# Optimization experiments

Hardware: AMD Instinct MI355X
Metric: run time of the kernel (lower is better)

## Reference

```python
import jax, jax.numpy as jnp
import numpy as np

# Fixed causal graph: 32 endo nodes, each with a private 16-dim exogenous parent.
# Nodes 0..3 are roots (no endo parents); node i>=4 has endo parents {i-4..i-1}.
N_NODES = 32
ENDO = 16      # endogenous features per node
EXO = 16       # exogenous features per node
HID = 64       # hidden width (module default hidden_features=[64,64])
N_ROOTS = 4
N_PAR = 4      # endo parents for non-root nodes
IN_ROOT = EXO                      # 16
IN_INNER = N_PAR * ENDO + EXO      # 80
BATCH = 32768


def _init(key, shape, fan_in):
    return jax.random.normal(key, shape, jnp.float32) * (1.0 / np.sqrt(fan_in))


def setup_inputs() -> dict:
    key = jax.random.key(0)
    ks = jax.random.split(key, 13)
    n_in = N_NODES - N_ROOTS
    return {
        "u": jax.random.normal(ks[0], (BATCH, N_NODES * EXO), jnp.float32),
        # stacked root MLPs: [n_roots, in, out]
        "w_r1": _init(ks[1], (N_ROOTS, IN_ROOT, HID), IN_ROOT),
        "b_r1": jnp.zeros((N_ROOTS, HID), jnp.float32),
        "w_r2": _init(ks[2], (N_ROOTS, HID, HID), HID),
        "b_r2": jnp.zeros((N_ROOTS, HID), jnp.float32),
        "w_r3": _init(ks[3], (N_ROOTS, HID, ENDO), HID),
        "b_r3": jnp.zeros((N_ROOTS, ENDO), jnp.float32),
        # stacked inner MLPs: [n_inner, in, out]
        "w_i1": _init(ks[4], (n_in, IN_INNER, HID), IN_INNER),
        "b_i1": jnp.zeros((n_in, HID), jnp.float32),
        "w_i2": _init(ks[5], (n_in, HID, HID), HID),
        "b_i2": jnp.zeros((n_in, HID), jnp.float32),
        "w_i3": _init(ks[6], (n_in, HID, ENDO), HID),
        "b_i3": jnp.zeros((n_in, ENDO), jnp.float32),
    }


def _mlp(x, w1, b1, w2, b2, w3, b3):
    h = jax.nn.relu(x @ w1 + b1)
    h = jax.nn.relu(h @ w2 + b2)
    return h @ w3 + b3


def reference(u, w_r1, b_r1, w_r2, b_r2, w_r3, b_r3,
              w_i1, b_i1, w_i2, b_i2, w_i3, b_i3):
    B = u.shape[0]
    U = u.reshape(B, N_NODES, EXO)  # per-node exogenous inputs
    # Root nodes: no endo parents, vectorized over the 4 roots.
    h = jax.nn.relu(jnp.einsum("bni,nio->bno", U[:, :N_ROOTS], w_r1) + b_r1)
    h = jax.nn.relu(jnp.einsum("bnh,nho->bno", h, w_r2) + b_r2)
    root_v = jnp.einsum("bnh,nhd->bnd", h, w_r3) + b_r3  # [B, 4, ENDO]
    V = [root_v[:, i] for i in range(N_ROOTS)]
    # Non-root nodes in topological order: gather thresholded parents -> MLP.
    for i in range(N_ROOTS, N_NODES):
        j = i - N_ROOTS
        parents = jnp.concatenate(
            [(V[p] > 0.5).astype(u.dtype) for p in range(i - N_PAR, i)], axis=-1)
        inp = jnp.concatenate([parents, U[:, i]], axis=-1)  # [B, 80]
        V.append(_mlp(inp, w_i1[j], b_i1[j], w_i2[j], b_i2[j], w_i3[j], b_i3[j]))
    # forward() uses soft=True, T/W_T/W_E=None -> E is the raw logits, batched.
    return jnp.concatenate(V, axis=-1)  # [B, N_NODES*ENDO]
```

## Files before the change

kernel.cpp:

```cpp
#include <hip/hip_runtime.h>


#define BT 64

typedef __attribute__((ext_vector_type(8))) short bf16x8;
typedef __attribute__((ext_vector_type(4))) float f32x4;
#define MFMA16 __builtin_amdgcn_mfma_f32_16x16x32_bf16

#define NODE_STRIDE 33792
#define W1_SPLIT    6144
#define W2_OFF      18432
#define W2_SPLIT    4096
#define W3_OFF      30720
#define W3_SPLIT    1024

__device__ inline unsigned short bf16_rne(float x) {
    unsigned u = __float_as_uint(x);
    u += 0x7fffu + ((u >> 16) & 1u);
    return (unsigned short)(u >> 16);
}
__device__ inline float bf16_tof(unsigned short h) {
    return __uint_as_float(((unsigned)h) << 16);
}
__device__ inline void split3(float x, unsigned short& h, unsigned short& m,
                              unsigned short& l) {
    h = bf16_rne(x);
    float r = x - bf16_tof(h);
    m = bf16_rne(r);
    float r2 = r - bf16_tof(m);
    l = bf16_rne(r2);
}

__device__ inline unsigned cvt_pk_bf16(float a, float b) {
    unsigned d;
    asm("v_cvt_pk_bf16_f32 %0, %1, %2" : "=v"(d) : "v"(a), "v"(b));
    return d;
}
__device__ inline void split3_pair(float a, float b,
                                   unsigned& h, unsigned& m, unsigned& l) {
    h = cvt_pk_bf16(a, b);
    float ra = a - __uint_as_float(h << 16);
    float rb = b - __uint_as_float(h & 0xffff0000u);
    m = cvt_pk_bf16(ra, rb);
    float sa = ra - __uint_as_float(m << 16);
    float sb = rb - __uint_as_float(m & 0xffff0000u);
    l = cvt_pk_bf16(sa, sb);
}

__device__ inline int hswz(int e, int feat) {
    return (feat & 7) | ((((feat >> 3) ^ e) & 7) << 3);
}

__device__ inline void bar_lgkm() {
    asm volatile("s_waitcnt lgkmcnt(0)\n\ts_barrier" ::: "memory");
}

#define PER_NODE_ITEMS (64 * 96 + 64 * 64 + 16 * 64)

__global__ void prep_weights(const float* __restrict__ w_r1,
                             const float* __restrict__ w_r2,
                             const float* __restrict__ w_r3,
                             const float* __restrict__ w_i1,
                             const float* __restrict__ w_i2,
                             const float* __restrict__ w_i3,
                             unsigned short* __restrict__ ws) {
    int tid = blockIdx.x * 256 + threadIdx.x;
    if (tid >= 32 * PER_NODE_ITEMS) return;
    int node = tid / PER_NODE_ITEMS;
    int r = tid - node * PER_NODE_ITEMS;
    int off, stride;
    float wv = 0.0f;
    if (r < 6144) {
        int n = r / 96, k = r - n * 96;
        if (k < 64) {
            wv = (node >= 4) ? w_i1[((node - 4) * 80 + k) * 64 + n] : 0.0f;
        } else if (k < 80) {
            wv = (node < 4) ? w_r1[(node * 16 + (k - 64)) * 64 + n]
                            : w_i1[((node - 4) * 80 + k) * 64 + n];
        }
        off = n * 96 + k; stride = W1_SPLIT;
    } else if (r < 10240) {
        int r2 = r - 6144;
        int n = r2 >> 6, k = r2 & 63;
        wv = (node < 4) ? w_r2[(node * 64 + k) * 64 + n]
                        : w_i2[((node - 4) * 64 + k) * 64 + n];
        off = W2_OFF + n * 64 + k; stride = W2_SPLIT;
    } else {
        int r3 = r - 10240;
        int n = r3 >> 6, k = r3 & 63;
        wv = (node < 4) ? w_r3[(node * 64 + k) * 16 + n]
                        : w_i3[((node - 4) * 64 + k) * 16 + n];
        off = W3_OFF + n * 64 + k; stride = W3_SPLIT;
    }
    unsigned short h, m, l;
    split3(wv, h, m, l);
    unsigned short* base = ws + node * NODE_STRIDE;
    base[off] = h;
    base[off + stride] = m;
    base[off + 2 * stride] = l;
}

#define LOAD_W1(nn) do {                                                      \
    const unsigned short* Wb_ = ws + (long)(nn) * NODE_STRIDE + n1 * 96;      \
    _Pragma("unroll") for (int g_ = 0; g_ < 2; ++g_) {                        \
        const unsigned short* wp_ = Wb_ + g_ * 32 + lq * 8;                   \
        w1f[g_ * 3 + 0] = *(const bf16x8*)(wp_);                              \
        w1f[g_ * 3 + 1] = *(const bf16x8*)(wp_ + W1_SPLIT);                   \
        w1f[g_ * 3 + 2] = *(const bf16x8*)(wp_ + 2 * W1_SPLIT);               \
    }                                                                         \
    const unsigned short* we_ = Wb_ + 64 + lq * 8;                            \
    w1f[6] = *(const bf16x8*)(we_);                                           \
    w1f[7] = *(const bf16x8*)(we_ + W1_SPLIT);                                \
    w1f[8] = *(const bf16x8*)(we_ + 2 * W1_SPLIT);                            \
} while (0)

#define LOAD_W2(nn) do {                                                      \
    const unsigned short* Wb_ =                                               \
        ws + (long)(nn) * NODE_STRIDE + W2_OFF + n1 * 64;                     \
    _Pragma("unroll") for (int g_ = 0; g_ < 2; ++g_) {                        \
        const unsigned short* wp_ = Wb_ + g_ * 32 + lq * 8;                   \
        w2f[g_ * 3 + 0] = *(const bf16x8*)(wp_);                              \
        w2f[g_ * 3 + 1] = *(const bf16x8*)(wp_ + W2_SPLIT);                   \
        w2f[g_ * 3 + 2] = *(const bf16x8*)(wp_ + 2 * W2_SPLIT);               \
    }                                                                         \
} while (0)

#define LOAD_W3(nn) do {                                                      \
    const unsigned short* Wb_ =                                               \
        ws + (long)(nn) * NODE_STRIDE + W3_OFF + lr * 64;                     \
    _Pragma("unroll") for (int g_ = 0; g_ < 2; ++g_) {                        \
        const unsigned short* wp_ = Wb_ + g_ * 32 + lq * 8;                   \
        w3f[g_ * 3 + 0] = *(const bf16x8*)(wp_);                              \
        w3f[g_ * 3 + 1] = *(const bf16x8*)(wp_ + W3_SPLIT);                   \
        w3f[g_ * 3 + 2] = *(const bf16x8*)(wp_ + 2 * W3_SPLIT);               \
    }                                                                         \
} while (0)

#define STAGE_XU(uv) do {                                                     \
    unsigned hS0_, mS0_, lS0_, hS1_, mS1_, lS1_;                              \
    split3_pair((uv).x, (uv).y, hS0_, mS0_, lS0_);                            \
    split3_pair((uv).z, (uv).w, hS1_, mS1_, lS1_);                            \
    *(uint2*)&xu[0][l][4 * w] = make_uint2(hS0_, hS1_);                       \
    *(uint2*)&xu[1][l][4 * w] = make_uint2(mS0_, mS1_);                       \
    *(uint2*)&xu[2][l][4 * w] = make_uint2(lS0_, lS1_);                       \
} while (0)

__global__ __launch_bounds__(256, 2) void ncm_mfma(
    const float* __restrict__ u,
    const unsigned short* __restrict__ ws,
    const float* __restrict__ b_r1, const float* __restrict__ b_r2,
    const float* __restrict__ b_r3, const float* __restrict__ b_i1,
    const float* __restrict__ b_i2, const float* __restrict__ b_i3,
    float* __restrict__ out)
{
    __shared__ __align__(16) unsigned short ring[4][64][24];
    __shared__ __align__(16) unsigned short xu[3][64][40];
    __shared__ __align__(16) unsigned short h1s[3][64][64];
    __shared__ __align__(16) unsigned short h2s[3][64][64];

    const int tid = threadIdx.x;
    const int l   = tid & 63;
    const int w   = tid >> 6;
    const int lr  = l & 15;
    const int lq  = l >> 4;
    const int n1  = 16 * w + lr;

    const long eg = (long)blockIdx.x * BT;
    const float* u_blk = u + eg * 512;

    bf16x8 w1f[9], w2f[6], w3f[6];

    LOAD_W1(0);
    LOAD_W2(0);
    {
        float4 uv = *(const float4*)(u_blk + (long)l * 512 + w * 4);
        STAGE_XU(uv);
    }
    bar_lgkm();

    for (int i = 0; i < 32; ++i) {
        const int nn = (i < 31) ? i + 1 : 31;
        f32x4 acc[4] = {{0,0,0,0},{0,0,0,0},{0,0,0,0},{0,0,0,0}};

        LOAD_W3(i);
        float4 uN;
        if (i < 31)
            uN = *(const float4*)(u_blk + (long)l * 512 + nn * 16 + w * 4);

        if (i >= 4) {
            #pragma unroll
            for (int g = 0; g < 2; ++g) {
                const int f = g * 32 + lq * 8;
                const int slot = (i + (f >> 4)) & 3;
                #pragma unroll
                for (int m = 0; m < 4; ++m) {
                    bf16x8 ab = *(const bf16x8*)&ring[slot][m * 16 + lr][f & 15];
                    acc[m] = MFMA16(w1f[g * 3 + 0], ab, acc[m], 0, 0, 0);
                    acc[m] = MFMA16(w1f[g * 3 + 1], ab, acc[m], 0, 0, 0);
                    acc[m] = MFMA16(w1f[g * 3 + 2], ab, acc[m], 0, 0, 0);
                }
            }
        }
        {
            #pragma unroll
            for (int m = 0; m < 4; ++m) {
                bf16x8 a0 = {}, a1 = {}, a2 = {};
                if (lq < 2) {
                    const int e = m * 16 + lr;
                    a0 = *(const bf16x8*)&xu[0][e][lq * 8];
                    a1 = *(const bf16x8*)&xu[1][e][lq * 8];
                    a2 = *(const bf16x8*)&xu[2][e][lq * 8];
                }
                acc[m] = MFMA16(w1f[6], a0, acc[m], 0, 0, 0);
                acc[m] = MFMA16(w1f[7], a0, acc[m], 0, 0, 0);
                acc[m] = MFMA16(w1f[8], a0, acc[m], 0, 0, 0);
                acc[m] = MFMA16(w1f[6], a1, acc[m], 0, 0, 0);
                acc[m] = MFMA16(w1f[7], a1, acc[m], 0, 0, 0);
                acc[m] = MFMA16(w1f[8], a1, acc[m], 0, 0, 0);
                acc[m] = MFMA16(w1f[6], a2, acc[m], 0, 0, 0);
                acc[m] = MFMA16(w1f[7], a2, acc[m], 0, 0, 0);
            }
        }
        {
            const float* B1 = (i < 4) ? (b_r1 + i * 64) : (b_i1 + (i - 4) * 64);
            float4 bv = *(const float4*)(B1 + 16 * w + 4 * lq);
            const int fo = 16 * w + 4 * lq;
            #pragma unroll
            for (int m = 0; m < 4; ++m) {
                const int e = m * 16 + lr;
                float v0 = fmaxf(acc[m][0] + bv.x, 0.0f);
                float v1 = fmaxf(acc[m][1] + bv.y, 0.0f);
                float v2 = fmaxf(acc[m][2] + bv.z, 0.0f);
                float v3 = fmaxf(acc[m][3] + bv.w, 0.0f);
                unsigned hP0, mP0, lP0, hP1, mP1, lP1;
                split3_pair(v0, v1, hP0, mP0, lP0);
                split3_pair(v2, v3, hP1, mP1, lP1);
                const int o = hswz(e, fo);
                *(uint2*)&h1s[0][e][o] = make_uint2(hP0, hP1);
                *(uint2*)&h1s[1][e][o] = make_uint2(mP0, mP1);
                *(uint2*)&h1s[2][e][o] = make_uint2(lP0, lP1);
            }
        }
        bar_lgkm();

        LOAD_W1(nn);
        if (i < 31) STAGE_XU(uN);

        #pragma unroll
        for (int m = 0; m < 4; ++m) acc[m] = (f32x4){0, 0, 0, 0};
        {
            #pragma unroll
            for (int g = 0; g < 2; ++g) {
                const int f = g * 32 + lq * 8;
                #pragma unroll
                for (int m = 0; m < 4; ++m) {
                    const int e = m * 16 + lr;
                    const int o = hswz(e, f);
                    bf16x8 a0 = *(const bf16x8*)&h1s[0][e][o];
                    bf16x8 a1 = *(const bf16x8*)&h1s[1][e][o];
                    bf16x8 a2 = *(const bf16x8*)&h1s[2][e][o];
                    acc[m] = MFMA16(w2f[g * 3 + 0], a0, acc[m], 0, 0, 0);
                    acc[m] = MFMA16(w2f[g * 3 + 1], a0, acc[m], 0, 0, 0);
                    acc[m] = MFMA16(w2f[g * 3 + 2], a0, acc[m], 0, 0, 0);
                    acc[m] = MFMA16(w2f[g * 3 + 0], a1, acc[m], 0, 0, 0);
                    acc[m] = MFMA16(w2f[g * 3 + 1], a1, acc[m], 0, 0, 0);
                    acc[m] = MFMA16(w2f[g * 3 + 2], a1, acc[m], 0, 0, 0);
                    acc[m] = MFMA16(w2f[g * 3 + 0], a2, acc[m], 0, 0, 0);
                    acc[m] = MFMA16(w2f[g * 3 + 1], a2, acc[m], 0, 0, 0);
                }
            }
        }
        {
            const float* B2 = (i < 4) ? (b_r2 + i * 64) : (b_i2 + (i - 4) * 64);
            float4 bv = *(const float4*)(B2 + 16 * w + 4 * lq);
            const int fo = 16 * w + 4 * lq;
            #pragma unroll
            for (int m = 0; m < 4; ++m) {
                const int e = m * 16 + lr;
                float v0 = fmaxf(acc[m][0] + bv.x, 0.0f);
                float v1 = fmaxf(acc[m][1] + bv.y, 0.0f);
                float v2 = fmaxf(acc[m][2] + bv.z, 0.0f);
                float v3 = fmaxf(acc[m][3] + bv.w, 0.0f);
                unsigned hP0, mP0, lP0, hP1, mP1, lP1;
                split3_pair(v0, v1, hP0, mP0, lP0);
                split3_pair(v2, v3, hP1, mP1, lP1);
                const int o = hswz(e, fo);
                *(uint2*)&h2s[0][e][o] = make_uint2(hP0, hP1);
                *(uint2*)&h2s[1][e][o] = make_uint2(mP0, mP1);
                *(uint2*)&h2s[2][e][o] = make_uint2(lP0, lP1);
            }
        }
        bar_lgkm();

        LOAD_W2(nn);
        {
            f32x4 c3 = {0, 0, 0, 0};
            const int e = 16 * w + lr;
            #pragma unroll
            for (int g = 0; g < 2; ++g) {
                const int f = g * 32 + lq * 8;
                const int o = hswz(e, f);
                bf16x8 a0 = *(const bf16x8*)&h2s[0][e][o];
                bf16x8 a1 = *(const bf16x8*)&h2s[1][e][o];
                bf16x8 a2 = *(const bf16x8*)&h2s[2][e][o];
                c3 = MFMA16(w3f[g * 3 + 0], a0, c3, 0, 0, 0);
                c3 = MFMA16(w3f[g * 3 + 1], a0, c3, 0, 0, 0);
                c3 = MFMA16(w3f[g * 3 + 2], a0, c3, 0, 0, 0);
                c3 = MFMA16(w3f[g * 3 + 0], a1, c3, 0, 0, 0);
                c3 = MFMA16(w3f[g * 3 + 1], a1, c3, 0, 0, 0);
                c3 = MFMA16(w3f[g * 3 + 2], a1, c3, 0, 0, 0);
                c3 = MFMA16(w3f[g * 3 + 0], a2, c3, 0, 0, 0);
                c3 = MFMA16(w3f[g * 3 + 1], a2, c3, 0, 0, 0);
            }
            const float* B3 = (i < 4) ? (b_r3 + i * 16) : (b_i3 + (i - 4) * 16);
            float4 bv = *(const float4*)(B3 + 4 * lq);
            float v0 = c3[0] + bv.x;
            float v1 = c3[1] + bv.y;
            float v2 = c3[2] + bv.z;
            float v3 = c3[3] + bv.w;
            *(float4*)(out + (eg + e) * 512 + i * 16 + 4 * lq) =
                make_float4(v0, v1, v2, v3);
            const int slot = i & 3;
            unsigned r0 = (v0 > 0.5f ? 0x3F80u : 0u) |
                          ((v1 > 0.5f ? 0x3F80u : 0u) << 16);
            unsigned r1 = (v2 > 0.5f ? 0x3F80u : 0u) |
                          ((v3 > 0.5f ? 0x3F80u : 0u) << 16);
            *(uint2*)&ring[slot][e][4 * lq] = make_uint2(r0, r1);
        }
        bar_lgkm();
    }
}

extern "C" void kernel_launch(void* const* d_in, const int* in_sizes, int n_in,
                              void* d_out, int out_size, void* d_ws, size_t ws_size,
                              hipStream_t stream) {
    const float* u    = (const float*)d_in[0];
    const float* w_r1 = (const float*)d_in[1];
    const float* b_r1 = (const float*)d_in[2];
    const float* w_r2 = (const float*)d_in[3];
    const float* b_r2 = (const float*)d_in[4];
    const float* w_r3 = (const float*)d_in[5];
    const float* b_r3 = (const float*)d_in[6];
    const float* w_i1 = (const float*)d_in[7];
    const float* b_i1 = (const float*)d_in[8];
    const float* w_i2 = (const float*)d_in[9];
    const float* b_i2 = (const float*)d_in[10];
    const float* w_i3 = (const float*)d_in[11];
    const float* b_i3 = (const float*)d_in[12];
    float* out = (float*)d_out;
    unsigned short* ws = (unsigned short*)d_ws;

    prep_weights<<<dim3((32 * PER_NODE_ITEMS) / 256), dim3(256), 0, stream>>>(
        w_r1, w_r2, w_r3, w_i1, w_i2, w_i3, ws);

    ncm_mfma<<<dim3(512), dim3(256), 0, stream>>>(
        u, ws, b_r1, b_r2, b_r3, b_i1, b_i2, b_i3, out);
}
```

Baseline: 284.4 us.

## Split batch rows across 8 waves per block instead of 4

Doubles the block to 512 threads. Waves are split into 4 output-column tiles times 2 batch-row halves, so each wave handles 2 row-tiles instead of 4 in layers 1 and 2. Layer 3 runs only on the first 4 waves, and each wave stages half as much exogenous input. The goal is more waves to hide MFMA and LDS latency, at the cost of duplicated weight-fragment loads per wave and idle waves during layer 3. The launch bound asks for 4 blocks per CU, which may force register pressure or spills.

New measurement: 376.0 us. 1.32x slower.

```diff
diff --git a/kernel.cpp b/kernel.cpp
--- a/kernel.cpp
+++ b/kernel.cpp
@@ -137,15 +137,14 @@
 } while (0)
 
 #define STAGE_XU(uv) do {                                                     \
-    unsigned hS0_, mS0_, lS0_, hS1_, mS1_, lS1_;                              \
-    split3_pair((uv).x, (uv).y, hS0_, mS0_, lS0_);                            \
-    split3_pair((uv).z, (uv).w, hS1_, mS1_, lS1_);                            \
-    *(uint2*)&xu[0][l][4 * w] = make_uint2(hS0_, hS1_);                       \
-    *(uint2*)&xu[1][l][4 * w] = make_uint2(mS0_, mS1_);                       \
-    *(uint2*)&xu[2][l][4 * w] = make_uint2(lS0_, lS1_);                       \
+    unsigned hS_, mS_, lS_;                                                   \
+    split3_pair((uv).x, (uv).y, hS_, mS_, lS_);                               \
+    *(unsigned*)&xu[0][l][2 * w8] = hS_;                                      \
+    *(unsigned*)&xu[1][l][2 * w8] = mS_;                                      \
+    *(unsigned*)&xu[2][l][2 * w8] = lS_;                                      \
 } while (0)
 
-__global__ __launch_bounds__(256, 2) void ncm_mfma(
+__global__ __launch_bounds__(512, 4) void ncm_mfma(
     const float* __restrict__ u,
     const unsigned short* __restrict__ ws,
     const float* __restrict__ b_r1, const float* __restrict__ b_r2,
@@ -160,10 +159,12 @@
 
     const int tid = threadIdx.x;
     const int l   = tid & 63;
-    const int w   = tid >> 6;
+    const int w8  = tid >> 6;
     const int lr  = l & 15;
     const int lq  = l >> 4;
-    const int n1  = 16 * w + lr;
+    const int nt  = w8 & 3;
+    const int mh  = w8 >> 2;
+    const int n1  = 16 * nt + lr;
 
     const long eg = (long)blockIdx.x * BT;
     const float* u_blk = u + eg * 512;
@@ -173,19 +174,19 @@
     LOAD_W1(0);
     LOAD_W2(0);
     {
-        float4 uv = *(const float4*)(u_blk + (long)l * 512 + w * 4);
+        float2 uv = *(const float2*)(u_blk + (long)l * 512 + 2 * w8);
         STAGE_XU(uv);
     }
     bar_lgkm();
 
     for (int i = 0; i < 32; ++i) {
         const int nn = (i < 31) ? i + 1 : 31;
-        f32x4 acc[4] = {{0,0,0,0},{0,0,0,0},{0,0,0,0},{0,0,0,0}};
-
-        LOAD_W3(i);
-        float4 uN;
+        f32x4 acc[2] = {{0,0,0,0},{0,0,0,0}};
+
+        if (w8 < 4) LOAD_W3(i);
+        float2 uN;
         if (i < 31)
-            uN = *(const float4*)(u_blk + (long)l * 512 + nn * 16 + w * 4);
+            uN = *(const float2*)(u_blk + (long)l * 512 + nn * 16 + 2 * w8);
 
         if (i >= 4) {
             #pragma unroll
@@ -193,8 +194,9 @@
                 const int f = g * 32 + lq * 8;
                 const int slot = (i + (f >> 4)) & 3;
                 #pragma unroll
-                for (int m = 0; m < 4; ++m) {
-                    bf16x8 ab = *(const bf16x8*)&ring[slot][m * 16 + lr][f & 15];
+                for (int m = 0; m < 2; ++m) {
+                    const int e = (2 * mh + m) * 16 + lr;
+                    bf16x8 ab = *(const bf16x8*)&ring[slot][e][f & 15];
                     acc[m] = MFMA16(w1f[g * 3 + 0], ab, acc[m], 0, 0, 0);
                     acc[m] = MFMA16(w1f[g * 3 + 1], ab, acc[m], 0, 0, 0);
                     acc[m] = MFMA16(w1f[g * 3 + 2], ab, acc[m], 0, 0, 0);
@@ -203,10 +205,10 @@
         }
         {
             #pragma unroll
-            for (int m = 0; m < 4; ++m) {
+            for (int m = 0; m < 2; ++m) {
                 bf16x8 a0 = {}, a1 = {}, a2 = {};
                 if (lq < 2) {
-                    const int e = m * 16 + lr;
+                    const int e = (2 * mh + m) * 16 + lr;
                     a0 = *(const bf16x8*)&xu[0][e][lq * 8];
                     a1 = *(const bf16x8*)&xu[1][e][lq * 8];
                     a2 = *(const bf16x8*)&xu[2][e][lq * 8];
@@ -223,11 +225,11 @@
         }
         {
             const float* B1 = (i < 4) ? (b_r1 + i * 64) : (b_i1 + (i - 4) * 64);
-            float4 bv = *(const float4*)(B1 + 16 * w + 4 * lq);
-            const int fo = 16 * w + 4 * lq;
-            #pragma unroll
-            for (int m = 0; m < 4; ++m) {
-                const int e = m * 16 + lr;
+            float4 bv = *(const float4*)(B1 + 16 * nt + 4 * lq);
+            const int fo = 16 * nt + 4 * lq;
+            #pragma unroll
+            for (int m = 0; m < 2; ++m) {
+                const int e = (2 * mh + m) * 16 + lr;
                 float v0 = fmaxf(acc[m][0] + bv.x, 0.0f);
                 float v1 = fmaxf(acc[m][1] + bv.y, 0.0f);
                 float v2 = fmaxf(acc[m][2] + bv.z, 0.0f);
@@ -247,14 +249,14 @@
         if (i < 31) STAGE_XU(uN);
 
         #pragma unroll
-        for (int m = 0; m < 4; ++m) acc[m] = (f32x4){0, 0, 0, 0};
+        for (int m = 0; m < 2; ++m) acc[m] = (f32x4){0, 0, 0, 0};
         {
             #pragma unroll
             for (int g = 0; g < 2; ++g) {
                 const int f = g * 32 + lq * 8;
                 #pragma unroll
-                for (int m = 0; m < 4; ++m) {
-                    const int e = m * 16 + lr;
+                for (int m = 0; m < 2; ++m) {
+                    const int e = (2 * mh + m) * 16 + lr;
                     const int o = hswz(e, f);
                     bf16x8 a0 = *(const bf16x8*)&h1s[0][e][o];
                     bf16x8 a1 = *(const bf16x8*)&h1s[1][e][o];
@@ -272,11 +274,11 @@
         }
         {
             const float* B2 = (i < 4) ? (b_r2 + i * 64) : (b_i2 + (i - 4) * 64);
-            float4 bv = *(const float4*)(B2 + 16 * w + 4 * lq);
-            const int fo = 16 * w + 4 * lq;
-            #pragma unroll
-            for (int m = 0; m < 4; ++m) {
-                const int e = m * 16 + lr;
+            float4 bv = *(const float4*)(B2 + 16 * nt + 4 * lq);
+            const int fo = 16 * nt + 4 * lq;
+            #pragma unroll
+            for (int m = 0; m < 2; ++m) {
+                const int e = (2 * mh + m) * 16 + lr;
                 float v0 = fmaxf(acc[m][0] + bv.x, 0.0f);
                 float v1 = fmaxf(acc[m][1] + bv.y, 0.0f);
                 float v2 = fmaxf(acc[m][2] + bv.z, 0.0f);
@@ -293,9 +295,9 @@
         bar_lgkm();
 
         LOAD_W2(nn);
-        {
+        if (w8 < 4) {
             f32x4 c3 = {0, 0, 0, 0};
-            const int e = 16 * w + lr;
+            const int e = 16 * w8 + lr;
             #pragma unroll
             for (int g = 0; g < 2; ++g) {
                 const int f = g * 32 + lq * 8;
@@ -353,6 +355,6 @@
     prep_weights<<<dim3((32 * PER_NODE_ITEMS) / 256), dim3(256), 0, stream>>>(
         w_r1, w_r2, w_r3, w_i1, w_i2, w_i3, ws);
 
-    ncm_mfma<<<dim3(512), dim3(256), 0, stream>>>(
+    ncm_mfma<<<dim3(512), dim3(512), 0, stream>>>(
         u, ws, b_r1, b_r2, b_r3, b_i1, b_i2, b_i3, out);
 }
```

## Make each wave own its batch rows in layer 2 to drop a barrier

Applied to the files above, without the earlier changes.

Layer 2 is repartitioned so each wave computes all 64 hidden outputs for its own 16 batch rows, instead of 16 outputs for all 64 rows. Layer 3 then reads only h2 rows the same wave wrote, so the block barrier between layer 2 and layer 3 is removed. The cost is holding all of W2 in registers per wave (24 bf16x8 fragments instead of 6), which raises register pressure and global weight load traffic and may lower occupancy.

New measurement: 420.4 us. +47.8%, slower.

```diff
diff --git a/kernel.cpp b/kernel.cpp
--- a/kernel.cpp
+++ b/kernel.cpp
@@ -115,13 +115,15 @@
 } while (0)
 
 #define LOAD_W2(nn) do {                                                      \
-    const unsigned short* Wb_ =                                               \
-        ws + (long)(nn) * NODE_STRIDE + W2_OFF + n1 * 64;                     \
-    _Pragma("unroll") for (int g_ = 0; g_ < 2; ++g_) {                        \
-        const unsigned short* wp_ = Wb_ + g_ * 32 + lq * 8;                   \
-        w2f[g_ * 3 + 0] = *(const bf16x8*)(wp_);                              \
-        w2f[g_ * 3 + 1] = *(const bf16x8*)(wp_ + W2_SPLIT);                   \
-        w2f[g_ * 3 + 2] = *(const bf16x8*)(wp_ + 2 * W2_SPLIT);               \
+    _Pragma("unroll") for (int nt_ = 0; nt_ < 4; ++nt_) {                     \
+        const unsigned short* Wb_ = ws + (long)(nn) * NODE_STRIDE + W2_OFF    \
+                                    + (nt_ * 16 + lr) * 64;                   \
+        _Pragma("unroll") for (int g_ = 0; g_ < 2; ++g_) {                    \
+            const unsigned short* wp_ = Wb_ + g_ * 32 + lq * 8;               \
+            w2f[nt_ * 6 + g_ * 3 + 0] = *(const bf16x8*)(wp_);                \
+            w2f[nt_ * 6 + g_ * 3 + 1] = *(const bf16x8*)(wp_ + W2_SPLIT);     \
+            w2f[nt_ * 6 + g_ * 3 + 2] = *(const bf16x8*)(wp_ + 2 * W2_SPLIT); \
+        }                                                                     \
     }                                                                         \
 } while (0)
 
@@ -164,11 +166,12 @@
     const int lr  = l & 15;
     const int lq  = l >> 4;
     const int n1  = 16 * w + lr;
+    const int e2  = 16 * w + lr;
 
     const long eg = (long)blockIdx.x * BT;
     const float* u_blk = u + eg * 512;
 
-    bf16x8 w1f[9], w2f[6], w3f[6];
+    bf16x8 w1f[9], w2f[24], w3f[6];
 
     LOAD_W1(0);
     LOAD_W2(0);
@@ -252,57 +255,51 @@
             #pragma unroll
             for (int g = 0; g < 2; ++g) {
                 const int f = g * 32 + lq * 8;
+                const int o = hswz(e2, f);
+                bf16x8 a0 = *(const bf16x8*)&h1s[0][e2][o];
+                bf16x8 a1 = *(const bf16x8*)&h1s[1][e2][o];
+                bf16x8 a2 = *(const bf16x8*)&h1s[2][e2][o];
                 #pragma unroll
-                for (int m = 0; m < 4; ++m) {
-                    const int e = m * 16 + lr;
-                    const int o = hswz(e, f);
-                    bf16x8 a0 = *(const bf16x8*)&h1s[0][e][o];
-                    bf16x8 a1 = *(const bf16x8*)&h1s[1][e][o];
-                    bf16x8 a2 = *(const bf16x8*)&h1s[2][e][o];
-                    acc[m] = MFMA16(w2f[g * 3 + 0], a0, acc[m], 0, 0, 0);
-                    acc[m] = MFMA16(w2f[g * 3 + 1], a0, acc[m], 0, 0, 0);
-                    acc[m] = MFMA16(w2f[g * 3 + 2], a0, acc[m], 0, 0, 0);
-                    acc[m] = MFMA16(w2f[g * 3 + 0], a1, acc[m], 0, 0, 0);
-                    acc[m] = MFMA16(w2f[g * 3 + 1], a1, acc[m], 0, 0, 0);
-                    acc[m] = MFMA16(w2f[g * 3 + 2], a1, acc[m], 0, 0, 0);
-                    acc[m] = MFMA16(w2f[g * 3 + 0], a2, acc[m], 0, 0, 0);
-                    acc[m] = MFMA16(w2f[g * 3 + 1], a2, acc[m], 0, 0, 0);
+                for (int nt = 0; nt < 4; ++nt) {
+                    acc[nt] = MFMA16(w2f[nt * 6 + g * 3 + 0], a0, acc[nt], 0, 0, 0);
+                    acc[nt] = MFMA16(w2f[nt * 6 + g * 3 + 1], a0, acc[nt], 0, 0, 0);
+                    acc[nt] = MFMA16(w2f[nt * 6 + g * 3 + 2], a0, acc[nt], 0, 0, 0);
+                    acc[nt] = MFMA16(w2f[nt * 6 + g * 3 + 0], a1, acc[nt], 0, 0, 0);
+                    acc[nt] = MFMA16(w2f[nt * 6 + g * 3 + 1], a1, acc[nt], 0, 0, 0);
+                    acc[nt] = MFMA16(w2f[nt * 6 + g * 3 + 2], a1, acc[nt], 0, 0, 0);
+                    acc[nt] = MFMA16(w2f[nt * 6 + g * 3 + 0], a2, acc[nt], 0, 0, 0);
+                    acc[nt] = MFMA16(w2f[nt * 6 + g * 3 + 1], a2, acc[nt], 0, 0, 0);
                 }
             }
         }
+        LOAD_W2(nn);
         {
             const float* B2 = (i < 4) ? (b_r2 + i * 64) : (b_i2 + (i - 4) * 64);
-            float4 bv = *(const float4*)(B2 + 16 * w + 4 * lq);
-            const int fo = 16 * w + 4 * lq;
-            #pragma unroll
-            for (int m = 0; m < 4; ++m) {
-                const int e = m * 16 + lr;
-                float v0 = fmaxf(acc[m][0] + bv.x, 0.0f);
-                float v1 = fmaxf(acc[m][1] + bv.y, 0.0f);
-                float v2 = fmaxf(acc[m][2] + bv.z, 0.0f);
-                float v3 = fmaxf(acc[m][3] + bv.w, 0.0f);
+            #pragma unroll
+            for (int nt = 0; nt < 4; ++nt) {
+                float4 bv = *(const float4*)(B2 + 16 * nt + 4 * lq);
+                float v0 = fmaxf(acc[nt][0] + bv.x, 0.0f);
+                float v1 = fmaxf(acc[nt][1] + bv.y, 0.0f);
+                float v2 = fmaxf(acc[nt][2] + bv.z, 0.0f);
+                float v3 = fmaxf(acc[nt][3] + bv.w, 0.0f);
                 unsigned hP0, mP0, lP0, hP1, mP1, lP1;
                 split3_pair(v0, v1, hP0, mP0, lP0);
                 split3_pair(v2, v3, hP1, mP1, lP1);
-                const int o = hswz(e, fo);
-                *(uint2*)&h2s[0][e][o] = make_uint2(hP0, hP1);
-                *(uint2*)&h2s[1][e][o] = make_uint2(mP0, mP1);
-                *(uint2*)&h2s[2][e][o] = make_uint2(lP0, lP1);
-            }
-        }
-        bar_lgkm();
-
-        LOAD_W2(nn);
+                const int o = hswz(e2, 16 * nt + 4 * lq);
+                *(uint2*)&h2s[0][e2][o] = make_uint2(hP0, hP1);
+                *(uint2*)&h2s[1][e2][o] = make_uint2(mP0, mP1);
+                *(uint2*)&h2s[2][e2][o] = make_uint2(lP0, lP1);
+            }
+        }
         {
             f32x4 c3 = {0, 0, 0, 0};
-            const int e = 16 * w + lr;
             #pragma unroll
             for (int g = 0; g < 2; ++g) {
                 const int f = g * 32 + lq * 8;
-                const int o = hswz(e, f);
-                bf16x8 a0 = *(const bf16x8*)&h2s[0][e][o];
-                bf16x8 a1 = *(const bf16x8*)&h2s[1][e][o];
-                bf16x8 a2 = *(const bf16x8*)&h2s[2][e][o];
+                const int o = hswz(e2, f);
+                bf16x8 a0 = *(const bf16x8*)&h2s[0][e2][o];
+                bf16x8 a1 = *(const bf16x8*)&h2s[1][e2][o];
+                bf16x8 a2 = *(const bf16x8*)&h2s[2][e2][o];
                 c3 = MFMA16(w3f[g * 3 + 0], a0, c3, 0, 0, 0);
                 c3 = MFMA16(w3f[g * 3 + 1], a0, c3, 0, 0, 0);
                 c3 = MFMA16(w3f[g * 3 + 2], a0, c3, 0, 0, 0);
@@ -318,14 +315,14 @@
             float v1 = c3[1] + bv.y;
             float v2 = c3[2] + bv.z;
             float v3 = c3[3] + bv.w;
-            *(float4*)(out + (eg + e) * 512 + i * 16 + 4 * lq) =
+            *(float4*)(out + (eg + e2) * 512 + i * 16 + 4 * lq) =
                 make_float4(v0, v1, v2, v3);
             const int slot = i & 3;
             unsigned r0 = (v0 > 0.5f ? 0x3F80u : 0u) |
                           ((v1 > 0.5f ? 0x3F80u : 0u) << 16);
             unsigned r1 = (v2 > 0.5f ? 0x3F80u : 0u) |
                           ((v3 > 0.5f ? 0x3F80u : 0u) << 16);
-            *(uint2*)&ring[slot][e][4 * lq] = make_uint2(r0, r1);
+            *(uint2*)&ring[slot][e2][4 * lq] = make_uint2(r0, r1);
         }
         bar_lgkm();
     }
```
